# Kernel optimization log

Measured on AMD Instinct MI355X. Metric: run time of the kernel, lower is better.

The kernel has to match this reference:

```python
import jax, jax.numpy as jnp
import numpy as np

N_NODES = 100000
SEQ = 16          # spiral length
IN_C = 3
NUM_CLASSES = 12


def _xavier(key, shape):
    fan_out, fan_in = shape
    limit = float(np.sqrt(6.0 / (fan_in + fan_out)))
    return jax.random.uniform(key, shape, jnp.float32, -limit, limit)


def setup_inputs() -> dict:
    key = jax.random.key(0)
    ks = jax.random.split(key, 8)
    x = jax.random.normal(ks[0], (N_NODES, IN_C), jnp.float32)
    indices = jax.random.randint(ks[1], (N_NODES, SEQ), 0, N_NODES, jnp.int64)
    return {
        "x": x,
        "indices": indices,
        "fc0_w": _xavier(ks[2], (16, IN_C)),
        "fc0_b": jnp.zeros((16,), jnp.float32),
        "w1": _xavier(ks[3], (32, 16 * SEQ)),
        "b1": jnp.zeros((32,), jnp.float32),
        "w2": _xavier(ks[4], (64, 32 * SEQ)),
        "b2": jnp.zeros((64,), jnp.float32),
        "w3": _xavier(ks[5], (128, 64 * SEQ)),
        "b3": jnp.zeros((128,), jnp.float32),
        "fc1_w": _xavier(ks[6], (256, 128)),
        "fc1_b": jnp.zeros((256,), jnp.float32),
        "fc2_w": _xavier(ks[7], (NUM_CLASSES, 256)),
        "fc2_b": jnp.zeros((NUM_CLASSES,), jnp.float32),
    }


def _spiral_conv(x, indices, w, b):
    # gather spiral neighborhoods: [N, S, C] -> [N, S*C], then linear
    n = indices.shape[0]
    g = x[indices.reshape(-1)].reshape(n, -1)
    return g @ w.T + b


def reference(x, indices, fc0_w, fc0_b, w1, b1, w2, b2, w3, b3,
              fc1_w, fc1_b, fc2_w, fc2_b):
    h = jax.nn.elu(x @ fc0_w.T + fc0_b)                 # [N, 16]
    h = jax.nn.elu(_spiral_conv(h, indices, w1, b1))    # [N, 32]
    h = jax.nn.elu(_spiral_conv(h, indices, w2, b2))    # [N, 64]
    h = jax.nn.elu(_spiral_conv(h, indices, w3, b3))    # [N, 128]
    h = jax.nn.elu(h @ fc1_w.T + fc1_b)                 # [N, 256]
    # dropout is identity in eval mode
    logits = h @ fc2_w.T + fc2_b                        # [N, num_classes]
    return jax.nn.log_softmax(logits, axis=1)
```

## Files before the change

kernel.cpp:

```cpp
#include <hip/hip_runtime.h>
#include <hip/hip_fp8.h>
#include <math.h>
#include <utility>


typedef __bf16 bf16x8 __attribute__((ext_vector_type(8)));
typedef float f32x16 __attribute__((ext_vector_type(16)));

template <int V> using ic = std::integral_constant<int, V>;

template <typename F, int... Is>
__device__ __forceinline__ void static_for_impl(F&& f, std::integer_sequence<int, Is...>) {
    (f(ic<Is>{}), ...);
}
template <int N_, typename F>
__device__ __forceinline__ void static_for(F&& f) {
    static_for_impl(static_cast<F&&>(f), std::make_integer_sequence<int, N_>{});
}

template <int N_>
__device__ __forceinline__ void wait_vmcnt() {
    static_assert(N_ <= 63, "vmcnt range");
    __builtin_amdgcn_s_waitcnt((N_ & 0xF) | (0x7 << 4) | (0xF << 8) | ((N_ >> 4) << 14));
}

__device__ __forceinline__ void memfence_sched() { __builtin_amdgcn_sched_barrier(0x000F); }

__device__ __forceinline__ float elu_f(float v) { return v > 0.f ? v : expm1f(v); }

__device__ __forceinline__ unsigned char to_fp8(float v) {
    __hip_fp8_e4m3 q(v);
    return (unsigned char)q.__x;
}

__device__ __forceinline__ bf16x8 dq8(long v) {
    bf16x8 r;
#pragma unroll
    for (int j = 0; j < 8; ++j) {
        __hip_fp8_e4m3 q;
        q.__x = (unsigned char)(v >> (8 * j));
        r[j] = (__bf16)(float)q;
    }
    return r;
}

template <int K, int C>
__device__ __forceinline__ void swz_one(const float* __restrict__ src, __bf16* __restrict__ dst, int j)
{
    int col = j / K;
    int k = j & (K - 1);
    int chunk = ((k >> 6) * 8 + ((k & 63) >> 3)) * C + col;
    dst[chunk * 8 + (k & 7)] = (__bf16)src[j];
}

__global__ __launch_bounds__(256) void cvt_swz_kernel(const float* __restrict__ w1,
                                                      const float* __restrict__ w2,
                                                      const float* __restrict__ w3,
                                                      const float* __restrict__ f1,
                                                      const float* __restrict__ f2,
                                                      __bf16* __restrict__ d1,
                                                      __bf16* __restrict__ d2,
                                                      __bf16* __restrict__ d3,
                                                      __bf16* __restrict__ df1,
                                                      __bf16* __restrict__ df2p)
{
    int i = blockIdx.x * 256 + threadIdx.x;
    if (i < 8192)        swz_one<256, 32>(w1, d1, i);
    else if (i < 40960)  swz_one<512, 64>(w2, d2, i - 8192);
    else if (i < 172032) swz_one<1024, 128>(w3, d3, i - 40960);
    else if (i < 204800) swz_one<128, 256>(f1, df1, i - 172032);
    else if (i < 212992) {
        int d = i - 204800;
        int e = d & 7;
        int chunkIdx = d >> 3;
        int col = chunkIdx & 31;
        int q = chunkIdx >> 5;
        int k = (q >> 3) * 64 + (q & 7) * 8 + e;
        df2p[d] = (col < 12) ? (__bf16)f2[col * 256 + k] : (__bf16)0.f;
    }
}

__global__ __launch_bounds__(256) void idxT_kernel(const int* __restrict__ idx,
                                                   int* __restrict__ idxT, int N)
{
    int i = blockIdx.x * 256 + threadIdx.x;
    if (i >= N * 16) return;
    int n = i >> 4, s = i & 15;
    idxT[s * N + n] = idx[i];
}

__global__ __launch_bounds__(256) void fc0_kernel(const float* __restrict__ x,
                                                  const float* __restrict__ w,
                                                  const float* __restrict__ b,
                                                  __bf16* __restrict__ h0, int N)
{
    int n = blockIdx.x * 256 + threadIdx.x;
    if (n >= N) return;
    float x0 = x[n * 3 + 0], x1 = x[n * 3 + 1], x2 = x[n * 3 + 2];
    __bf16 ob[16];
#pragma unroll
    for (int j = 0; j < 16; ++j)
        ob[j] = (__bf16)elu_f(w[j * 3 + 0] * x0 + w[j * 3 + 1] * x1 + w[j * 3 + 2] * x2 + b[j]);
    int4* dst = (int4*)&h0[(size_t)n * 16];
    dst[0] = *(int4*)&ob[0];
    dst[1] = *(int4*)&ob[8];
}

template <int CIN, int S, int COUT_B, int COUT_TOT, int TILE_M, int RW, int CW,
          bool GATHER, bool OUTF8, int MINW, int NN>
__global__ __launch_bounds__(256, MINW) void mfma_layer(const __bf16* __restrict__ hin,
                                                        const int* __restrict__ idxT,
                                                        const __bf16* __restrict__ Wsw,
                                                        const float* __restrict__ bias,
                                                        void* __restrict__ hout)
{
    constexpr int K = CIN * S;
    constexpr int NSTEP = K / 64;
    static_assert(K % 64 == 0, "K%64");
    constexpr int WM = TILE_M / RW;
    constexpr int WN = COUT_B / CW;
    constexpr int MT = WM / 32;
    constexpr int NT = WN / 32;
    constexpr int IPS = GATHER ? (64 / CIN) : 1;
    constexpr int D = WM / 8;
    constexpr int Bn = NT * 4;
    constexpr int I = GATHER ? D : 0;
    constexpr int NBUFS = 2;
    static_assert(RW * CW == 4, "4 waves");
    static_assert(WM == 32 || WM == 64, "1-2 row subtiles per wave");

    constexpr int AB = 4 * NBUFS * WM * 128;
    constexpr int CB = OUTF8 ? TILE_M * (COUT_B + 16) : TILE_M * (COUT_B + 8) * 2;
    constexpr int SH = AB > CB ? AB : CB;
    __shared__ __align__(16) char smem[SH];

    const int tid = threadIdx.x;
    const int lane = tid & 63;
    const int w = tid >> 6;
    const int wr = w / CW;
    const int wc = w % CW;
    const int ml = lane & 31;
    const int kh = lane >> 5;
    const int m0 = blockIdx.x * TILE_M;
    const int col0 = blockIdx.y * COUT_B;
    const int rbase = m0 + wr * WM;

    char* const Aw = smem + w * (NBUFS * WM * 128);

    int ioff[GATHER ? D : 1];
    int koff[GATHER ? D : 1];
    int gmr[GATHER ? 1 : D];
    int coff[GATHER ? 1 : D];
#pragma unroll
    for (int i = 0; i < D; ++i) {
        int r = i * 8 + (lane >> 3);
        int c = (lane & 7) ^ (r & 7);
        int gm = rbase + r; if (gm >= NN) gm = NN - 1;
        if constexpr (GATHER) {
            ioff[i] = ((c * 8) / CIN) * NN + gm;
            koff[i] = (c * 8) & (CIN - 1);
        } else {
            gmr[i] = gm;
            coff[i] = c * 8;
        }
    }

    bf16x8 bfr[2][NT][4];
    int myIdx[GATHER ? 3 : 1][GATHER ? D : 1];

    const __bf16* wlane = Wsw + ((size_t)(col0 + wc * WN + ml) + (size_t)kh * COUT_TOT) * 8;

    auto loadB = [&](auto sc) {
        constexpr int s = decltype(sc)::value;
        if constexpr (s < NSTEP) {
#pragma unroll
            for (int ni = 0; ni < NT; ++ni)
#pragma unroll
                for (int ks = 0; ks < 4; ++ks)
                    bfr[s & 1][ni][ks] = *(const bf16x8*)(wlane
                        + (size_t)(s * 8 + ks * 2) * COUT_TOT * 8 + ni * 32 * 8);
        }
    };
    auto loadIdxS = [&](auto sc) {
        constexpr int s = decltype(sc)::value;
        if constexpr (GATHER && s < NSTEP) {
#pragma unroll
            for (int i = 0; i < D; ++i)
                myIdx[s % 3][i] = idxT[(s * IPS) * NN + ioff[i]];
        }
    };
    auto issueDMA = [&](auto sc) {
        constexpr int s = decltype(sc)::value;
        if constexpr (s < NSTEP) {
            char* base = Aw + (s % NBUFS) * (WM * 128);
#pragma unroll
            for (int i = 0; i < D; ++i) {
                const __bf16* src;
                if constexpr (GATHER)
                    src = hin + (size_t)myIdx[s % 3][i] * CIN + koff[i];
                else
                    src = hin + (size_t)gmr[i] * K + s * 64 + coff[i];
                __builtin_amdgcn_global_load_lds(
                    (const __attribute__((address_space(1))) void*)src,
                    (__attribute__((address_space(3))) void*)(base + i * 1024),
                    16, 0, 0);
            }
        }
    };

    f32x16 acc[MT][NT];
#pragma unroll
    for (int mi = 0; mi < MT; ++mi)
#pragma unroll
        for (int ni = 0; ni < NT; ++ni) { f32x16 z = {}; acc[mi][ni] = z; }

    loadIdxS(ic<0>{});
    loadIdxS(ic<1>{});
    memfence_sched();
    loadB(ic<0>{});
    memfence_sched();
    issueDMA(ic<0>{});
    memfence_sched();
    loadIdxS(ic<2>{});
    memfence_sched();

    static_for<NSTEP>([&](auto sc) {
        constexpr int s = decltype(sc)::value;
        loadB(ic<s + 1>{});
        memfence_sched();
        issueDMA(ic<s + 1>{});
        memfence_sched();
        loadIdxS(ic<s + 3>{});
        memfence_sched();
        constexpr int NW = I * (s + 2 < NSTEP) + (Bn + D) * (s + 1 < NSTEP)
                         + I * (s + 3 < NSTEP);
        wait_vmcnt<NW>();
        memfence_sched();

        const char* base = Aw + (s % NBUFS) * (WM * 128);
        bf16x8 afr[MT][4];
#pragma unroll
        for (int mi = 0; mi < MT; ++mi)
#pragma unroll
            for (int ks = 0; ks < 4; ++ks) {
                int cb = ks * 2 + kh;
                afr[mi][ks] = *(const bf16x8*)(base + ((mi * 32 + ml) * 8 + (cb ^ (ml & 7))) * 16);
            }
#pragma unroll
        for (int ks = 0; ks < 4; ++ks)
#pragma unroll
            for (int mi = 0; mi < MT; ++mi)
#pragma unroll
                for (int ni = 0; ni < NT; ++ni)
                    acc[mi][ni] = __builtin_amdgcn_mfma_f32_32x32x16_bf16(
                        afr[mi][ks], bfr[s & 1][ni][ks], acc[mi][ni], 0, 0, 0);
    });

    __syncthreads();
    if constexpr (OUTF8) {
        unsigned char* Cs8 = (unsigned char*)smem;
        constexpr int LDC8 = COUT_B + 16;
#pragma unroll
        for (int ni = 0; ni < NT; ++ni) {
            const int col = wc * WN + ni * 32 + ml;
            const float bv = bias[col0 + col];
#pragma unroll
            for (int mi = 0; mi < MT; ++mi) {
#pragma unroll
                for (int r = 0; r < 16; ++r) {
                    int row = wr * WM + mi * 32 + ((r & 3) + 8 * (r >> 2) + 4 * kh);
                    Cs8[row * LDC8 + col] = to_fp8(elu_f(acc[mi][ni][r] + bv));
                }
            }
        }
        __syncthreads();
        constexpr int C16 = COUT_B / 16;
#pragma unroll
        for (int j2 = tid; j2 < TILE_M * C16; j2 += 256) {
            int row = j2 / C16, c16 = j2 % C16;
            int gm = m0 + row;
            if (gm < NN)
                *(int4*)((unsigned char*)hout + (size_t)gm * COUT_TOT + col0 + c16 * 16)
                    = *(int4*)&Cs8[row * LDC8 + c16 * 16];
        }
    } else {
        __bf16* Cs = (__bf16*)smem;
        constexpr int LDC = COUT_B + 8;
#pragma unroll
        for (int ni = 0; ni < NT; ++ni) {
            const int col = wc * WN + ni * 32 + ml;
            const float bv = bias[col0 + col];
#pragma unroll
            for (int mi = 0; mi < MT; ++mi) {
#pragma unroll
                for (int r = 0; r < 16; ++r) {
                    int row = wr * WM + mi * 32 + ((r & 3) + 8 * (r >> 2) + 4 * kh);
                    Cs[row * LDC + col] = (__bf16)elu_f(acc[mi][ni][r] + bv);
                }
            }
        }
        __syncthreads();
        constexpr int C8 = COUT_B / 8;
#pragma unroll
        for (int j2 = tid; j2 < TILE_M * C8; j2 += 256) {
            int row = j2 / C8, c8 = j2 % C8;
            int gm = m0 + row;
            if (gm < NN)
                *(int4*)&((__bf16*)hout)[(size_t)gm * COUT_TOT + col0 + c8 * 8] = *(int4*)&Cs[row * LDC + c8 * 8];
        }
    }
}

__global__ __launch_bounds__(256, 3) void mfma3_mixed(const unsigned char* __restrict__ h2f8,
                                                      const int* __restrict__ idxT,
                                                      const __bf16* __restrict__ Wsw,
                                                      const float* __restrict__ bias,
                                                      __bf16* __restrict__ h3)
{
    constexpr int NN = 100000;
    constexpr int NSTEP = 16;
    constexpr int D = 2;
    constexpr int Bn = 8;
    constexpr int I = 2;
    __shared__ __align__(16) char smem[17408];

    const int tid = threadIdx.x;
    const int lane = tid & 63;
    const int w = tid >> 6;
    const int wr = w >> 1;
    const int wc = w & 1;
    const int ml = lane & 31;
    const int kh = lane >> 5;
    const int m0 = blockIdx.x * 64;
    const int rbase = m0 + wr * 32;

    char* const Aw = smem + w * 4096;

    int ioff[D], koff[D];
#pragma unroll
    for (int i = 0; i < D; ++i) {
        int r = i * 16 + (lane >> 2);
        int c = (lane & 3) ^ (r & 3);
        int gm = rbase + r; if (gm >= NN) gm = NN - 1;
        ioff[i] = gm;
        koff[i] = c * 16;
    }

    bf16x8 bfr[2][2][4];
    int myIdx[3][D];

    const __bf16* wlane = Wsw + ((size_t)(wc * 64 + ml) + (size_t)kh * 128) * 8;

    auto loadB = [&](auto sc) {
        constexpr int s = decltype(sc)::value;
        if constexpr (s < NSTEP) {
#pragma unroll
            for (int ni = 0; ni < 2; ++ni)
#pragma unroll
                for (int ks = 0; ks < 4; ++ks)
                    bfr[s & 1][ni][ks] = *(const bf16x8*)(wlane
                        + (size_t)(s * 8 + ks * 2) * 128 * 8 + ni * 32 * 8);
        }
    };
    auto loadIdxS = [&](auto sc) {
        constexpr int s = decltype(sc)::value;
        if constexpr (s < NSTEP) {
#pragma unroll
            for (int i = 0; i < D; ++i)
                myIdx[s % 3][i] = idxT[(size_t)s * NN + ioff[i]];
        }
    };
    auto issueDMA = [&](auto sc) {
        constexpr int s = decltype(sc)::value;
        if constexpr (s < NSTEP) {
            char* base = Aw + (s & 1) * 2048;
#pragma unroll
            for (int i = 0; i < D; ++i) {
                const unsigned char* src = h2f8 + (size_t)myIdx[s % 3][i] * 64 + koff[i];
                __builtin_amdgcn_global_load_lds(
                    (const __attribute__((address_space(1))) void*)src,
                    (__attribute__((address_space(3))) void*)(base + i * 1024),
                    16, 0, 0);
            }
        }
    };

    f32x16 acc[2];
    { f32x16 z = {}; acc[0] = z; acc[1] = z; }

    loadIdxS(ic<0>{});
    loadIdxS(ic<1>{});
    memfence_sched();
    loadB(ic<0>{});
    memfence_sched();
    issueDMA(ic<0>{});
    memfence_sched();
    loadIdxS(ic<2>{});
    memfence_sched();

    static_for<NSTEP>([&](auto sc) {
        constexpr int s = decltype(sc)::value;
        loadB(ic<s + 1>{});
        memfence_sched();
        issueDMA(ic<s + 1>{});
        memfence_sched();
        loadIdxS(ic<s + 3>{});
        memfence_sched();
        constexpr int NW = I * (s + 2 < NSTEP) + (Bn + D) * (s + 1 < NSTEP)
                         + I * (s + 3 < NSTEP);
        wait_vmcnt<NW>();
        memfence_sched();

        const char* base = Aw + (s & 1) * 2048;
        bf16x8 afr[4];
#pragma unroll
        for (int ks = 0; ks < 4; ++ks) {
            long a8 = *(const long*)(base + ml * 64 + ((ks ^ (ml & 3)) << 4) + kh * 8);
            afr[ks] = dq8(a8);
        }
#pragma unroll
        for (int ks = 0; ks < 4; ++ks)
#pragma unroll
            for (int ni = 0; ni < 2; ++ni)
                acc[ni] = __builtin_amdgcn_mfma_f32_32x32x16_bf16(
                    afr[ks], bfr[s & 1][ni][ks], acc[ni], 0, 0, 0);
    });

    __syncthreads();
    __bf16* Cs = (__bf16*)smem;
#pragma unroll
    for (int ni = 0; ni < 2; ++ni) {
        const int col = wc * 64 + ni * 32 + ml;
        const float bv = bias[col];
#pragma unroll
        for (int r = 0; r < 16; ++r) {
            int row = wr * 32 + ((r & 3) + 8 * (r >> 2) + 4 * kh);
            Cs[row * 136 + col] = (__bf16)elu_f(acc[ni][r] + bv);
        }
    }
    __syncthreads();
#pragma unroll
    for (int j2 = tid; j2 < 64 * 16; j2 += 256) {
        int row = j2 >> 4, c8 = j2 & 15;
        int gm = m0 + row;
        if (gm < NN)
            *(int4*)&h3[(size_t)gm * 128 + c8 * 8] = *(int4*)&Cs[row * 136 + c8 * 8];
    }
}

__global__ __launch_bounds__(256, 3) void fc12_kernel(const __bf16* __restrict__ h3,
                                                      const __bf16* __restrict__ Wsw,
                                                      const float* __restrict__ bias1,
                                                      const __bf16* __restrict__ W2p,
                                                      const float* __restrict__ bias2,
                                                      float* __restrict__ out)
{
    __shared__ __align__(16) char smem[32 * 264 * 2];
    const int tid = threadIdx.x;
    const int lane = tid & 63;
    const int w = tid >> 6;
    const int ml = lane & 31;
    const int kh = lane >> 5;
    const int m0 = blockIdx.x * 32;

    const __bf16* wlane = Wsw + ((size_t)(w * 64 + ml) + (size_t)kh * 256) * 8;
    bf16x8 bfr[2][2][4];
#pragma unroll
    for (int s = 0; s < 2; ++s)
#pragma unroll
        for (int ni = 0; ni < 2; ++ni)
#pragma unroll
            for (int ks = 0; ks < 4; ++ks)
                bfr[s][ni][ks] = *(const bf16x8*)(wlane
                    + (size_t)(s * 8 + ks * 2) * 256 * 8 + ni * 32 * 8);

    bf16x8 b2f[4];
#pragma unroll
    for (int ks = 0; ks < 4; ++ks)
        b2f[ks] = *(const bf16x8*)&W2p[((w * 8 + ks * 2 + kh) * 32 + ml) * 8];

#pragma unroll
    for (int t = 0; t < 2; ++t) {
        int j = w * 2 + t;
        int lr = j * 4 + (lane >> 4);
        int sc = (lane & 15) ^ (lr & 15);
        const __bf16* src = h3 + (size_t)(m0 + lr) * 128 + sc * 8;
        __builtin_amdgcn_global_load_lds(
            (const __attribute__((address_space(1))) void*)src,
            (__attribute__((address_space(3))) void*)(smem + j * 1024),
            16, 0, 0);
    }
    wait_vmcnt<0>();
    __syncthreads();

    f32x16 acc[2];
    { f32x16 z = {}; acc[0] = z; acc[1] = z; }
    const char* Ab = smem;
#pragma unroll
    for (int s = 0; s < 2; ++s) {
        bf16x8 afr[4];
#pragma unroll
        for (int ks = 0; ks < 4; ++ks) {
            int c16 = s * 8 + ks * 2 + kh;
            afr[ks] = *(const bf16x8*)(Ab + ml * 256 + ((c16 ^ (ml & 15)) * 16));
        }
#pragma unroll
        for (int ks = 0; ks < 4; ++ks)
#pragma unroll
            for (int ni = 0; ni < 2; ++ni)
                acc[ni] = __builtin_amdgcn_mfma_f32_32x32x16_bf16(afr[ks], bfr[s][ni][ks], acc[ni], 0, 0, 0);
    }
    __syncthreads();

    __bf16* Cs = (__bf16*)smem;
#pragma unroll
    for (int ni = 0; ni < 2; ++ni) {
        int col = w * 64 + ni * 32 + ml;
        float bv = bias1[col];
#pragma unroll
        for (int r = 0; r < 16; ++r) {
            int row = (r & 3) + 8 * (r >> 2) + 4 * kh;
            Cs[row * 264 + col] = (__bf16)elu_f(acc[ni][r] + bv);
        }
    }
    __syncthreads();

    bf16x8 a2[4];
#pragma unroll
    for (int ks = 0; ks < 4; ++ks)
        a2[ks] = *(const bf16x8*)&Cs[ml * 264 + w * 64 + ks * 16 + kh * 8];
    f32x16 acc2;
    { f32x16 z = {}; acc2 = z; }
#pragma unroll
    for (int ks = 0; ks < 4; ++ks)
        acc2 = __builtin_amdgcn_mfma_f32_32x32x16_bf16(a2[ks], b2f[ks], acc2, 0, 0, 0);
    __syncthreads();

    float* P = (float*)(smem + w * 4096);
#pragma unroll
    for (int r = 0; r < 16; ++r)
        P[((r & 3) + 8 * (r >> 2) + 4 * kh) * 32 + ml] = acc2[r];
    __syncthreads();

    float4 s4 = make_float4(0.f, 0.f, 0.f, 0.f);
#pragma unroll
    for (int pw = 0; pw < 4; ++pw) {
        float4 v = *(float4*)(smem + pw * 4096 + tid * 16);
        s4.x += v.x; s4.y += v.y; s4.z += v.z; s4.w += v.w;
    }
    __syncthreads();
    *(float4*)(smem + tid * 16) = s4;
    __syncthreads();

    if (tid < 32) {
        const float* L = (float*)smem + tid * 32;
        float logits[12], mx = -1e30f;
#pragma unroll
        for (int o = 0; o < 12; ++o) {
            logits[o] = L[o] + bias2[o];
            mx = fmaxf(mx, logits[o]);
        }
        float s = 0.f;
#pragma unroll
        for (int o = 0; o < 12; ++o) s += expf(logits[o] - mx);
        float lse = mx + logf(s);
        int n = m0 + tid;
        float4 o0 = make_float4(logits[0] - lse, logits[1] - lse, logits[2] - lse, logits[3] - lse);
        float4 o1 = make_float4(logits[4] - lse, logits[5] - lse, logits[6] - lse, logits[7] - lse);
        float4 o2 = make_float4(logits[8] - lse, logits[9] - lse, logits[10] - lse, logits[11] - lse);
        *(float4*)&out[(size_t)n * 12 + 0] = o0;
        *(float4*)&out[(size_t)n * 12 + 4] = o1;
        *(float4*)&out[(size_t)n * 12 + 8] = o2;
    }
}

extern "C" void kernel_launch(void* const* d_in, const int* in_sizes, int n_in,
                              void* d_out, int out_size, void* d_ws, size_t ws_size,
                              hipStream_t stream)
{
    const int N = 100000;
    const float* x     = (const float*)d_in[0];
    const int*   idx   = (const int*)  d_in[1];
    const float* fc0_w = (const float*)d_in[2];
    const float* fc0_b = (const float*)d_in[3];
    const float* w1    = (const float*)d_in[4];
    const float* b1    = (const float*)d_in[5];
    const float* w2    = (const float*)d_in[6];
    const float* b2    = (const float*)d_in[7];
    const float* w3    = (const float*)d_in[8];
    const float* b3    = (const float*)d_in[9];
    const float* fc1_w = (const float*)d_in[10];
    const float* fc1_b = (const float*)d_in[11];
    const float* fc2_w = (const float*)d_in[12];
    const float* fc2_b = (const float*)d_in[13];
    float* out = (float*)d_out;

    char* ws = (char*)d_ws;
    const int n_w1 = 32 * 256, n_w2 = 64 * 512, n_w3 = 128 * 1024, n_fc1 = 256 * 128;
    const int n_fc2p = 32 * 256;
    const int n_wb = n_w1 + n_w2 + n_w3 + n_fc1 + n_fc2p;
    __bf16* w1b = (__bf16*)ws;
    __bf16* w2b = w1b + n_w1;
    __bf16* w3b = w2b + n_w2;
    __bf16* f1b = w3b + n_w3;
    __bf16* f2b = f1b + n_fc1;
    size_t off = ((size_t)n_wb * 2 + 4095) & ~(size_t)4095;
    int* idxT = (int*)(ws + off);              off += (size_t)N * 16 * 4;
    __bf16* h0 = (__bf16*)(ws + off);          off += (size_t)N * 16 * 2;
    __bf16* h1 = (__bf16*)(ws + off);          off += (size_t)N * 32 * 2;
    unsigned char* h2f8 = (unsigned char*)(ws + off);  off += (size_t)N * 64;
    __bf16* h3 = (__bf16*)(ws + off);          off += (size_t)N * 128 * 2;

    cvt_swz_kernel<<<(n_wb + 255) / 256, 256, 0, stream>>>(w1, w2, w3, fc1_w, fc2_w,
                                                           w1b, w2b, w3b, f1b, f2b);
    idxT_kernel<<<(N * 16 + 255) / 256, 256, 0, stream>>>(idx, idxT, N);
    fc0_kernel<<<(N + 255) / 256, 256, 0, stream>>>(x, fc0_w, fc0_b, h0, N);

    mfma_layer<16, 16, 32, 32, 128, 4, 1, true, false, 3, 100000>
        <<<dim3((N + 127) / 128, 1), 256, 0, stream>>>(h0, idxT, w1b, b1, (void*)h1);
    mfma_layer<32, 16, 64, 64, 128, 4, 1, true, true, 3, 100000>
        <<<dim3((N + 127) / 128, 1), 256, 0, stream>>>(h1, idxT, w2b, b2, (void*)h2f8);
    mfma3_mixed<<<(N + 63) / 64, 256, 0, stream>>>(h2f8, idxT, w3b, b3, h3);
    fc12_kernel<<<N / 32, 256, 0, stream>>>(h3, f1b, fc1_b, f2b, fc2_b, out);
}
```

Before: 226.3 us.

## Run spiral layer 3 with fp8 MFMA using split-residual fp8 weights

Layer-3 weights are stored as two fp8 parts, a main quantized value plus a scaled residual. The kernel then runs native fp8×fp8 MFMAs on the gathered fp8 activations instead of dequantizing them to bf16 in registers, and adds the two accumulators together in the epilogue. The LDS A-tile layout is changed to a simpler unswizzled arrangement that suits the fp8 fragment reads. This removes the per-element fp8→bf16 conversion work, but doubles the MFMA count, and occupancy drops from 3 to 2 blocks per CU because of the extra accumulators. The plain layout may also bring LDS bank conflicts.

```diff
diff --git a/kernel.cpp b/kernel.cpp
--- a/kernel.cpp
+++ b/kernel.cpp
@@ -6,6 +6,7 @@
 
 typedef __bf16 bf16x8 __attribute__((ext_vector_type(8)));
 typedef float f32x16 __attribute__((ext_vector_type(16)));
+typedef long long2v __attribute__((ext_vector_type(2)));
 
 template <int V> using ic = std::integral_constant<int, V>;
 
@@ -32,16 +33,10 @@
     __hip_fp8_e4m3 q(v);
     return (unsigned char)q.__x;
 }
-
-__device__ __forceinline__ bf16x8 dq8(long v) {
-    bf16x8 r;
-#pragma unroll
-    for (int j = 0; j < 8; ++j) {
-        __hip_fp8_e4m3 q;
-        q.__x = (unsigned char)(v >> (8 * j));
-        r[j] = (__bf16)(float)q;
-    }
-    return r;
+__device__ __forceinline__ float fp8_to_f(unsigned char b) {
+    __hip_fp8_e4m3 q;
+    q.__x = b;
+    return (float)q;
 }
 
 template <int K, int C>
@@ -60,23 +55,33 @@
                                                       const float* __restrict__ f2,
                                                       __bf16* __restrict__ d1,
                                                       __bf16* __restrict__ d2,
-                                                      __bf16* __restrict__ d3,
                                                       __bf16* __restrict__ df1,
-                                                      __bf16* __restrict__ df2p)
+                                                      __bf16* __restrict__ df2p,
+                                                      unsigned char* __restrict__ dw3)
 {
     int i = blockIdx.x * 256 + threadIdx.x;
     if (i < 8192)        swz_one<256, 32>(w1, d1, i);
     else if (i < 40960)  swz_one<512, 64>(w2, d2, i - 8192);
-    else if (i < 172032) swz_one<1024, 128>(w3, d3, i - 40960);
-    else if (i < 204800) swz_one<128, 256>(f1, df1, i - 172032);
-    else if (i < 212992) {
-        int d = i - 204800;
+    else if (i < 73728)  swz_one<128, 256>(f1, df1, i - 40960);
+    else if (i < 81920) {
+        int d = i - 73728;
         int e = d & 7;
         int chunkIdx = d >> 3;
         int col = chunkIdx & 31;
         int q = chunkIdx >> 5;
         int k = (q >> 3) * 64 + (q & 7) * 8 + e;
         df2p[d] = (col < 12) ? (__bf16)f2[col * 256 + k] : (__bf16)0.f;
+    } else if (i < 212992) {
+        int j = i - 81920;
+        int col = j >> 10;
+        int k = j & 1023;
+        float w = w3[j];
+        unsigned char q8 = to_fp8(w);
+        float r = 16.f * (w - fp8_to_f(q8));
+        unsigned char r8 = to_fp8(r);
+        size_t base = ((size_t)((k >> 3) * 128 + col)) * 16 + (k & 7);
+        dw3[base] = q8;
+        dw3[base + 8] = r8;
     }
 }
 
@@ -311,11 +316,11 @@
     }
 }
 
-__global__ __launch_bounds__(256, 3) void mfma3_mixed(const unsigned char* __restrict__ h2f8,
-                                                      const int* __restrict__ idxT,
-                                                      const __bf16* __restrict__ Wsw,
-                                                      const float* __restrict__ bias,
-                                                      __bf16* __restrict__ h3)
+__global__ __launch_bounds__(256, 2) void mfma3_dual(const unsigned char* __restrict__ h2f8,
+                                                     const int* __restrict__ idxT,
+                                                     const unsigned char* __restrict__ W3d,
+                                                     const float* __restrict__ bias,
+                                                     __bf16* __restrict__ h3)
 {
     constexpr int NN = 100000;
     constexpr int NSTEP = 16;
@@ -336,20 +341,19 @@
 
     char* const Aw = smem + w * 4096;
 
-    int ioff[D], koff[D];
+    int ioff[D], koff;
 #pragma unroll
     for (int i = 0; i < D; ++i) {
-        int r = i * 16 + (lane >> 2);
-        int c = (lane & 3) ^ (r & 3);
-        int gm = rbase + r; if (gm >= NN) gm = NN - 1;
+        int gm = rbase + i * 16 + (lane & 15);
+        if (gm >= NN) gm = NN - 1;
         ioff[i] = gm;
-        koff[i] = c * 16;
-    }
-
-    bf16x8 bfr[2][2][4];
+    }
+    koff = (lane >> 4) * 16;
+
+    long2v bqr[2][2][4];
     int myIdx[3][D];
 
-    const __bf16* wlane = Wsw + ((size_t)(wc * 64 + ml) + (size_t)kh * 128) * 8;
+    const unsigned char* wlane = W3d + ((size_t)(wc * 64 + ml) + (size_t)kh * 128) * 16;
 
     auto loadB = [&](auto sc) {
         constexpr int s = decltype(sc)::value;
@@ -358,8 +362,8 @@
             for (int ni = 0; ni < 2; ++ni)
 #pragma unroll
                 for (int ks = 0; ks < 4; ++ks)
-                    bfr[s & 1][ni][ks] = *(const bf16x8*)(wlane
-                        + (size_t)(s * 8 + ks * 2) * 128 * 8 + ni * 32 * 8);
+                    bqr[s & 1][ni][ks] = *(const long2v*)(wlane
+                        + (size_t)(s * 8 + ks * 2) * 2048 + ni * 512);
         }
     };
     auto loadIdxS = [&](auto sc) {
@@ -376,7 +380,7 @@
             char* base = Aw + (s & 1) * 2048;
 #pragma unroll
             for (int i = 0; i < D; ++i) {
-                const unsigned char* src = h2f8 + (size_t)myIdx[s % 3][i] * 64 + koff[i];
+                const unsigned char* src = h2f8 + (size_t)myIdx[s % 3][i] * 64 + koff;
                 __builtin_amdgcn_global_load_lds(
                     (const __attribute__((address_space(1))) void*)src,
                     (__attribute__((address_space(3))) void*)(base + i * 1024),
@@ -385,8 +389,8 @@
         }
     };
 
-    f32x16 acc[2];
-    { f32x16 z = {}; acc[0] = z; acc[1] = z; }
+    f32x16 accq[2], accr[2];
+    { f32x16 z = {}; accq[0] = z; accq[1] = z; accr[0] = z; accr[1] = z; }
 
     loadIdxS(ic<0>{});
     loadIdxS(ic<1>{});
@@ -411,19 +415,20 @@
         wait_vmcnt<NW>();
         memfence_sched();
 
-        const char* base = Aw + (s & 1) * 2048;
-        bf16x8 afr[4];
-#pragma unroll
-        for (int ks = 0; ks < 4; ++ks) {
-            long a8 = *(const long*)(base + ml * 64 + ((ks ^ (ml & 3)) << 4) + kh * 8);
-            afr[ks] = dq8(a8);
-        }
+        const char* base = Aw + (s & 1) * 2048 + (ml >> 4) * 1024 + (ml & 15) * 16 + kh * 8;
+        long afr[4];
 #pragma unroll
         for (int ks = 0; ks < 4; ++ks)
-#pragma unroll
-            for (int ni = 0; ni < 2; ++ni)
-                acc[ni] = __builtin_amdgcn_mfma_f32_32x32x16_bf16(
-                    afr[ks], bfr[s & 1][ni][ks], acc[ni], 0, 0, 0);
+            afr[ks] = *(const long*)(base + ks * 256);
+#pragma unroll
+        for (int ks = 0; ks < 4; ++ks)
+#pragma unroll
+            for (int ni = 0; ni < 2; ++ni) {
+                accq[ni] = __builtin_amdgcn_mfma_f32_32x32x16_fp8_fp8(
+                    afr[ks], bqr[s & 1][ni][ks].x, accq[ni], 0, 0, 0);
+                accr[ni] = __builtin_amdgcn_mfma_f32_32x32x16_fp8_fp8(
+                    afr[ks], bqr[s & 1][ni][ks].y, accr[ni], 0, 0, 0);
+            }
     });
 
     __syncthreads();
@@ -435,7 +440,8 @@
 #pragma unroll
         for (int r = 0; r < 16; ++r) {
             int row = wr * 32 + ((r & 3) + 8 * (r >> 2) + 4 * kh);
-            Cs[row * 136 + col] = (__bf16)elu_f(acc[ni][r] + bv);
+            float v = accq[ni][r] + 0.0625f * accr[ni][r] + bv;
+            Cs[row * 136 + col] = (__bf16)elu_f(v);
         }
     }
     __syncthreads();
@@ -596,23 +602,21 @@
     float* out = (float*)d_out;
 
     char* ws = (char*)d_ws;
-    const int n_w1 = 32 * 256, n_w2 = 64 * 512, n_w3 = 128 * 1024, n_fc1 = 256 * 128;
-    const int n_fc2p = 32 * 256;
-    const int n_wb = n_w1 + n_w2 + n_w3 + n_fc1 + n_fc2p;
+    const int n_w1 = 32 * 256, n_w2 = 64 * 512, n_fc1 = 256 * 128, n_fc2p = 32 * 256;
     __bf16* w1b = (__bf16*)ws;
     __bf16* w2b = w1b + n_w1;
-    __bf16* w3b = w2b + n_w2;
-    __bf16* f1b = w3b + n_w3;
+    __bf16* f1b = w2b + n_w2;
     __bf16* f2b = f1b + n_fc1;
-    size_t off = ((size_t)n_wb * 2 + 4095) & ~(size_t)4095;
+    unsigned char* w3d = (unsigned char*)(f2b + n_fc2p);
+    size_t off = (((size_t)(n_w1 + n_w2 + n_fc1 + n_fc2p) * 2 + 262144) + 4095) & ~(size_t)4095;
     int* idxT = (int*)(ws + off);              off += (size_t)N * 16 * 4;
     __bf16* h0 = (__bf16*)(ws + off);          off += (size_t)N * 16 * 2;
     __bf16* h1 = (__bf16*)(ws + off);          off += (size_t)N * 32 * 2;
     unsigned char* h2f8 = (unsigned char*)(ws + off);  off += (size_t)N * 64;
     __bf16* h3 = (__bf16*)(ws + off);          off += (size_t)N * 128 * 2;
 
-    cvt_swz_kernel<<<(n_wb + 255) / 256, 256, 0, stream>>>(w1, w2, w3, fc1_w, fc2_w,
-                                                           w1b, w2b, w3b, f1b, f2b);
+    cvt_swz_kernel<<<(212992 + 255) / 256, 256, 0, stream>>>(w1, w2, w3, fc1_w, fc2_w,
+                                                             w1b, w2b, f1b, f2b, w3d);
     idxT_kernel<<<(N * 16 + 255) / 256, 256, 0, stream>>>(idx, idxT, N);
     fc0_kernel<<<(N + 255) / 256, 256, 0, stream>>>(x, fc0_w, fc0_b, h0, N);
 
@@ -620,6 +624,6 @@
         <<<dim3((N + 127) / 128, 1), 256, 0, stream>>>(h0, idxT, w1b, b1, (void*)h1);
     mfma_layer<32, 16, 64, 64, 128, 4, 1, true, true, 3, 100000>
         <<<dim3((N + 127) / 128, 1), 256, 0, stream>>>(h1, idxT, w2b, b2, (void*)h2f8);
-    mfma3_mixed<<<(N + 63) / 64, 256, 0, stream>>>(h2f8, idxT, w3b, b3, h3);
+    mfma3_dual<<<(N + 63) / 64, 256, 0, stream>>>(h2f8, idxT, w3d, b3, h3);
     fc12_kernel<<<N / 32, 256, 0, stream>>>(h3, f1b, fc1_b, f2b, fc2_b, out);
 }
```

Measured after the change: 237.2 us. +4.8%, slower.
